# Kernel tuning notes

Hardware: AMD Instinct MI355X
Metric: run time of the kernel (lower is better)

The kernel has to match this reference:

```python
import jax, jax.numpy as jnp
import numpy as np

ALPHA = 0.5  # leakage
T, B, I, H = 512, 64, 128, 1024
SCALE = 0.9  # input_scaling
RHO = 0.99   # target spectral radius (approximated by 1/sqrt(H) normal scaling)


def setup_inputs() -> dict:
    key = jax.random.key(0)
    k1, k2, k3, k4, k5 = jax.random.split(key, 5)
    x = jax.random.normal(k1, (T, B, I), dtype=jnp.float32)
    # uniform(-scale, scale) kernel init
    W_in0 = jax.random.uniform(k2, (H, I), jnp.float32, -SCALE, SCALE)
    # normal recurrent init scaled so spectral radius ~= rho (circular law: radius ~ sigma*sqrt(H))
    W_hat0 = jax.random.normal(k3, (H, H), jnp.float32) * (RHO / np.sqrt(H))
    W_in1 = jax.random.uniform(k4, (H, H), jnp.float32, -SCALE, SCALE)
    W_hat1 = jax.random.normal(k5, (H, H), jnp.float32) * (RHO / np.sqrt(H))
    return {"x": x, "W_in0": W_in0, "W_hat0": W_hat0, "W_in1": W_in1, "W_hat1": W_hat1}


def _run_layer(inp, W_in, W_hat):
    # inp: [T, B, F_in]; returns full state trajectory [T, B, H]
    def step(h, x_t):
        pre = x_t @ W_in.T + h @ W_hat.T          # [B, H]
        h_new = (1.0 - ALPHA) * h + ALPHA * jnp.tanh(pre)
        return h_new, h_new

    h0 = jnp.zeros((inp.shape[1], W_hat.shape[0]), dtype=inp.dtype)
    _, ys = jax.lax.scan(step, h0, inp)
    return ys


def reference(x, W_in0, W_hat0, W_in1, W_hat1):
    e0 = _run_layer(x, W_in0, W_hat0)   # layer 0 states [T, B, H]
    e1 = _run_layer(e0, W_in1, W_hat1)  # layer 1 states [T, B, H]
    return jnp.stack([e0, e1], axis=-2)  # [T, B, num_layers, H]
```

## Files before the change

### kernel.cpp

```cpp
#include <hip/hip_runtime.h>
#include <math.h>

#define TSTEPS 512
#define BATCH  64
#define HDIM   1024
#define IDIM   128
#define NBLOCKS 256
#define NTHR   512

typedef __attribute__((ext_vector_type(8))) short bf16x8;
typedef __attribute__((ext_vector_type(4))) float f32x4;
typedef __attribute__((ext_vector_type(4))) unsigned u32x4;

#define WI0HI 0
#define WI0LO (WI0HI + 1024*128)
#define WH0HI (WI0LO + 1024*128)
#define WH0LO (WH0HI + 1024*1024)
#define WI1HI (WH0LO + 1024*1024)
#define WI1LO (WI1HI + 1024*1024)
#define WH1HI (WI1LO + 1024*1024)
#define WH1LO (WH1HI + 1024*1024)
#define WS_USHORTS (WH1LO + 1024*1024)
#define CNT_OFF_BYTES ((size_t)WS_USHORTS * 2)
#define FLG_DW (256 * 16)
#define BAR_BYTES (2 * 256 * 64)

__device__ __forceinline__ unsigned short bf_hi(float f) {
    unsigned u = __builtin_bit_cast(unsigned, f);
    unsigned r = u + 0x7fffu + ((u >> 16) & 1u);
    return (unsigned short)(r >> 16);
}
__device__ __forceinline__ float bf_tof(unsigned short h) {
    unsigned u = ((unsigned)h) << 16;
    return __builtin_bit_cast(float, u);
}

__device__ __forceinline__ void split8v(f32x4 a, f32x4 b,
                                        bf16x8& ah, bf16x8& al) {
    float fv[8] = {a[0], a[1], a[2], a[3], b[0], b[1], b[2], b[3]};
    u32x4 H, L;
    #pragma unroll
    for (int q = 0; q < 4; ++q) {
        const float f0 = fv[2 * q], f1 = fv[2 * q + 1];
        unsigned h;
        asm("v_cvt_pk_bf16_f32 %0, %1, %2" : "=v"(h) : "v"(f0), "v"(f1));
        const float h0 = __builtin_bit_cast(float, h << 16);
        const float h1 = __builtin_bit_cast(float, h & 0xffff0000u);
        unsigned lo;
        asm("v_cvt_pk_bf16_f32 %0, %1, %2" : "=v"(lo) : "v"(f0 - h0), "v"(f1 - h1));
        H[q] = h; L[q] = lo;
    }
    ah = __builtin_bit_cast(bf16x8, H);
    al = __builtin_bit_cast(bf16x8, L);
}

__device__ __forceinline__ void ks_r2(f32x4 a, f32x4 b,
                                      bf16x8 bh, bf16x8 bl, f32x4& acc) {
    bf16x8 ah, al;
    split8v(a, b, ah, al);
    acc = __builtin_amdgcn_mfma_f32_16x16x32_bf16(ah, bh, acc, 0, 0, 0);
    acc = __builtin_amdgcn_mfma_f32_16x16x32_bf16(al, bh, acc, 0, 0, 0);
    acc = __builtin_amdgcn_mfma_f32_16x16x32_bf16(ah, bl, acc, 0, 0, 0);
}

#define LDG4(B, base, g) _Pragma("unroll") for (int c = 0; c < 4; ++c) { \
    (B)[2*c]   = *(const f32x4*)((base) + ((g)*4 + c) * 32); \
    (B)[2*c+1] = *(const f32x4*)((base) + ((g)*4 + c) * 32 + 4); }
#define PROC4(B, wOff, g) _Pragma("unroll") for (int c = 0; c < 4; ++c) { \
    ks_r2((B)[2*c], (B)[2*c+1], wfh[(wOff)+(g)*4+c], wfl[(wOff)+(g)*4+c], \
          ((((g)*4+c) & 1) ? accA : accB)); }

__global__ void prep_kernel(const float* __restrict__ Wi0, const float* __restrict__ Wh0,
                            const float* __restrict__ Wi1, const float* __restrict__ Wh1,
                            unsigned short* __restrict__ wsU)
{
    const int n = 1024*128 + 3*1024*1024;
    for (int e = blockIdx.x * blockDim.x + threadIdx.x; e < n;
         e += gridDim.x * blockDim.x) {
        const float* src; int idx, hiOff, loOff;
        if (e < 1024*128)            { src = Wi0; idx = e;              hiOff = WI0HI; loOff = WI0LO; }
        else if (e < 1024*128 + 1024*1024)   { src = Wh0; idx = e - 1024*128;   hiOff = WH0HI; loOff = WH0LO; }
        else if (e < 1024*128 + 2*1024*1024) { src = Wi1; idx = e - 1024*128 - 1024*1024; hiOff = WI1HI; loOff = WI1LO; }
        else                         { src = Wh1; idx = e - 1024*128 - 2*1024*1024; hiOff = WH1HI; loOff = WH1LO; }
        float f = src[idx];
        unsigned short h = bf_hi(f);
        wsU[hiOff + idx] = h;
        wsU[loOff + idx] = bf_hi(f - bf_tof(h));
    }
}

__device__ __forceinline__ void barrier_arrive(unsigned* cnt, unsigned epoch) {
    __syncthreads();
    if (threadIdx.x == 0)
        __hip_atomic_store(cnt + (unsigned)blockIdx.x * 16, epoch,
                           __ATOMIC_RELAXED, __HIP_MEMORY_SCOPE_AGENT);
}
__device__ __forceinline__ void barrier_wait(unsigned* cnt, unsigned epoch) {
    const int tid = (int)threadIdx.x;
    if (blockIdx.x == 0) {
        if (tid < 64) {
            unsigned* flg = cnt + FLG_DW;
            for (;;) {
                unsigned v0 = __hip_atomic_load(cnt + (tid      ) * 16, __ATOMIC_RELAXED, __HIP_MEMORY_SCOPE_AGENT);
                unsigned v1 = __hip_atomic_load(cnt + (tid +  64) * 16, __ATOMIC_RELAXED, __HIP_MEMORY_SCOPE_AGENT);
                unsigned v2 = __hip_atomic_load(cnt + (tid + 128) * 16, __ATOMIC_RELAXED, __HIP_MEMORY_SCOPE_AGENT);
                unsigned v3 = __hip_atomic_load(cnt + (tid + 192) * 16, __ATOMIC_RELAXED, __HIP_MEMORY_SCOPE_AGENT);
                bool ok = (v0 >= epoch) & (v1 >= epoch) & (v2 >= epoch) & (v3 >= epoch);
                if (__ballot(ok) == ~0ull) break;
                __builtin_amdgcn_s_sleep(1);
            }
            #pragma unroll
            for (int q = 0; q < 4; ++q)
                __hip_atomic_store(flg + (q * 64 + tid) * 16, epoch,
                                   __ATOMIC_RELAXED, __HIP_MEMORY_SCOPE_AGENT);
        }
    } else if (tid == 0) {
        unsigned* myflag = cnt + FLG_DW + (unsigned)blockIdx.x * 16;
        while (__hip_atomic_load(myflag, __ATOMIC_RELAXED,
                                 __HIP_MEMORY_SCOPE_AGENT) < epoch)
            __builtin_amdgcn_s_sleep(1);
    }
    __syncthreads();
}

__global__ __launch_bounds__(NTHR, 2) void reservoir_kernel(
    const float* __restrict__ x, float* __restrict__ out,
    const unsigned short* __restrict__ wsU, unsigned* __restrict__ cnt)
{
    __shared__ f32x4 red[8 * 64];

    const int bid = blockIdx.x;
    const int layer = bid >> 7;
    const int rr  = bid & 127;
    const int jt  = rr >> 1, mh = rr & 1;
    const int tid = (int)threadIdx.x;
    const int w   = __builtin_amdgcn_readfirstlane(tid >> 6);
    const int m2  = w & 1, kh = w >> 1;
    const int l   = tid & 63, lr = l & 15, tq = l >> 4;
    const int jbase = jt * 16;
    const int arow  = mh * 32 + m2 * 16 + lr;

    bf16x8 wfh[16], wfl[16];
    if (layer == 0) {
        const size_t rx = (size_t)(jbase + lr) * IDIM + kh * 32 + tq * 8;
        wfh[0] = *(const bf16x8*)(wsU + WI0HI + rx);
        wfl[0] = *(const bf16x8*)(wsU + WI0LO + rx);
        const size_t rh = (size_t)(jbase + lr) * HDIM + kh * 256 + tq * 8;
        #pragma unroll
        for (int ks = 0; ks < 8; ++ks) {
            wfh[1 + ks] = *(const bf16x8*)(wsU + WH0HI + rh + ks * 32);
            wfl[1 + ks] = *(const bf16x8*)(wsU + WH0LO + rh + ks * 32);
        }
    } else {
        const int hiOff = (kh < 2) ? WI1HI : WH1HI;
        const int loOff = (kh < 2) ? WI1LO : WH1LO;
        const size_t ro = (size_t)(jbase + lr) * HDIM + (kh & 1) * 512 + tq * 8;
        #pragma unroll
        for (int ks = 0; ks < 16; ++ks) {
            wfh[ks] = *(const bf16x8*)(wsU + hiOff + ro + ks * 32);
            wfl[ks] = *(const bf16x8*)(wsU + loOff + ro + ks * 32);
        }
    }

    float hold[4] = {0.f, 0.f, 0.f, 0.f};
    f32x4 accX = {0.f, 0.f, 0.f, 0.f};

    for (int i = 0; i <= TSTEPS; ++i) {
        const int t = layer ? (i - 1) : i;
        const bool valid = layer ? (t >= 0) : (t < TSTEPS);
        if (valid) {
            f32x4 accA = {0.f, 0.f, 0.f, 0.f};
            f32x4 accB = {0.f, 0.f, 0.f, 0.f};
            if (layer == 0) {
                if (i == 0) {
                    f32x4 xa = *(const f32x4*)(x + (size_t)t * (BATCH * IDIM) + arow * IDIM + kh * 32 + tq * 8);
                    f32x4 xb = *(const f32x4*)(x + (size_t)t * (BATCH * IDIM) + arow * IDIM + kh * 32 + tq * 8 + 4);
                    ks_r2(xa, xb, wfh[0], wfl[0], accA);
                } else {
                    accA = accX;
                }
                if (t >= 1) {
                    const float* h0 = out + (size_t)(t - 1) * 131072 + arow * 2048
                                      + kh * 256 + tq * 8;
                    f32x4 bA[8], bB[8];
                    LDG4(bA, h0, 0);
                    LDG4(bB, h0, 1);
                    PROC4(bA, 1, 0);
                    PROC4(bB, 1, 1);
                }
            } else {
                const bool doit = (kh < 2) || (t >= 1);
                if (doit) {
                    const int ts  = (kh < 2) ? t : (t - 1);
                    const float* src = out + (size_t)ts * 131072 + arow * 2048
                                       + ((kh < 2) ? 0 : 1024) + (kh & 1) * 512 + tq * 8;
                    f32x4 bA[8], bB[8];
                    LDG4(bA, src, 0);
                    LDG4(bB, src, 1);
                    PROC4(bA, 0, 0);
                    LDG4(bA, src, 2);
                    PROC4(bB, 0, 1);
                    LDG4(bB, src, 3);
                    PROC4(bA, 0, 2);
                    PROC4(bB, 0, 3);
                }
            }

            red[w * 64 + l] = accA + accB;
            __syncthreads();
            if (w < 2) {
                f32x4 s  = red[(w + 0) * 64 + l];
                f32x4 s1 = red[(w + 2) * 64 + l];
                f32x4 s2 = red[(w + 4) * 64 + l];
                f32x4 s3 = red[(w + 6) * 64 + l];
                #pragma unroll
                for (int r = 0; r < 4; ++r) {
                    const float pre = ((s[r] + s1[r]) + (s2[r] + s3[r]));
                    const float hnew = 0.5f * hold[r] + 0.5f * tanhf(pre);
                    hold[r] = hnew;
                    const int row = mh * 32 + w * 16 + tq * 4 + r;
                    const int col = jbase + lr;
                    float* dst = out + (size_t)t * 131072 + row * 2048 + layer * 1024 + col;
                    __hip_atomic_store(dst, hnew, __ATOMIC_RELAXED, __HIP_MEMORY_SCOPE_AGENT);
                }
            }
            __syncthreads();
        }
        if (i < TSTEPS) {
            barrier_arrive(cnt, (unsigned)(i + 1));
            if (layer == 0 && (i + 1) < TSTEPS) {
                const float* xs = x + (size_t)(i + 1) * (BATCH * IDIM) + arow * IDIM + kh * 32 + tq * 8;
                f32x4 xa = *(const f32x4*)(xs);
                f32x4 xb = *(const f32x4*)(xs + 4);
                f32x4 z = {0.f, 0.f, 0.f, 0.f};
                ks_r2(xa, xb, wfh[0], wfl[0], z);
                accX = z;
            }
            barrier_wait(cnt, (unsigned)(i + 1));
        }
    }
}

extern "C" void kernel_launch(void* const* d_in, const int* in_sizes, int n_in,
                              void* d_out, int out_size, void* d_ws, size_t ws_size,
                              hipStream_t stream) {
    const float* x   = (const float*)d_in[0];
    const float* Wi0 = (const float*)d_in[1];
    const float* Wh0 = (const float*)d_in[2];
    const float* Wi1 = (const float*)d_in[3];
    const float* Wh1 = (const float*)d_in[4];
    float* out = (float*)d_out;
    unsigned short* wsU = (unsigned short*)d_ws;
    unsigned* cnt = (unsigned*)((char*)d_ws + CNT_OFF_BYTES);

    hipMemsetAsync((char*)d_ws + CNT_OFF_BYTES, 0, BAR_BYTES, stream);
    prep_kernel<<<256, 256, 0, stream>>>(Wi0, Wh0, Wi1, Wh1, wsU);

    void* args[] = {(void*)&x, (void*)&out, (void*)&wsU, (void*)&cnt};
    hipLaunchCooperativeKernel((const void*)reservoir_kernel,
                               dim3(NBLOCKS), dim3(NTHR), args, 0, stream);
}
```

Before: 4.723 ms.

## Split grid barrier per layer and spread epilogue across all threads

Replaces the single global barrier with two per-layer barriers. Block 0 of each layer gathers arrivals only from its own 128 blocks and publishes to a separate flag array. Layer-1 blocks wait on both the layer-0 and layer-1 flags, so layer-0 blocks no longer wait for layer-1 stragglers. The reduction and tanh epilogue now runs on all 512 threads, one output element each, instead of two waves handling four each, which shortens the serial tail of every step. The price is extra flag memory and a more involved dependency protocol between the layers.

```diff
diff --git a/kernel.cpp b/kernel.cpp
--- a/kernel.cpp
+++ b/kernel.cpp
@@ -23,7 +23,7 @@
 #define WS_USHORTS (WH1LO + 1024*1024)
 #define CNT_OFF_BYTES ((size_t)WS_USHORTS * 2)
 #define FLG_DW (256 * 16)
-#define BAR_BYTES (2 * 256 * 64)
+#define BAR_BYTES (3 * 256 * 64)
 
 __device__ __forceinline__ unsigned short bf_hi(float f) {
     unsigned u = __builtin_bit_cast(unsigned, f);
@@ -95,30 +95,46 @@
         __hip_atomic_store(cnt + (unsigned)blockIdx.x * 16, epoch,
                            __ATOMIC_RELAXED, __HIP_MEMORY_SCOPE_AGENT);
 }
-__device__ __forceinline__ void barrier_wait(unsigned* cnt, unsigned epoch) {
+__device__ __forceinline__ void barrier_wait(unsigned* cnt, unsigned epoch, int layer) {
     const int tid = (int)threadIdx.x;
-    if (blockIdx.x == 0) {
+    const int bid = (int)blockIdx.x;
+    if ((bid & 127) == 0) {
         if (tid < 64) {
-            unsigned* flg = cnt + FLG_DW;
+            unsigned* arr = cnt + layer * (128 * 16);
             for (;;) {
-                unsigned v0 = __hip_atomic_load(cnt + (tid      ) * 16, __ATOMIC_RELAXED, __HIP_MEMORY_SCOPE_AGENT);
-                unsigned v1 = __hip_atomic_load(cnt + (tid +  64) * 16, __ATOMIC_RELAXED, __HIP_MEMORY_SCOPE_AGENT);
-                unsigned v2 = __hip_atomic_load(cnt + (tid + 128) * 16, __ATOMIC_RELAXED, __HIP_MEMORY_SCOPE_AGENT);
-                unsigned v3 = __hip_atomic_load(cnt + (tid + 192) * 16, __ATOMIC_RELAXED, __HIP_MEMORY_SCOPE_AGENT);
-                bool ok = (v0 >= epoch) & (v1 >= epoch) & (v2 >= epoch) & (v3 >= epoch);
+                unsigned v0 = __hip_atomic_load(arr + (tid     ) * 16, __ATOMIC_RELAXED, __HIP_MEMORY_SCOPE_AGENT);
+                unsigned v1 = __hip_atomic_load(arr + (tid + 64) * 16, __ATOMIC_RELAXED, __HIP_MEMORY_SCOPE_AGENT);
+                bool ok = (v0 >= epoch) & (v1 >= epoch);
                 if (__ballot(ok) == ~0ull) break;
                 __builtin_amdgcn_s_sleep(1);
             }
+            unsigned* flg = cnt + FLG_DW + layer * 4096;
             #pragma unroll
             for (int q = 0; q < 4; ++q)
                 __hip_atomic_store(flg + (q * 64 + tid) * 16, epoch,
                                    __ATOMIC_RELAXED, __HIP_MEMORY_SCOPE_AGENT);
         }
+        if (layer == 1 && tid == 0) {
+            unsigned* f0 = cnt + FLG_DW + (unsigned)bid * 16;
+            while (__hip_atomic_load(f0, __ATOMIC_RELAXED,
+                                     __HIP_MEMORY_SCOPE_AGENT) < epoch)
+                __builtin_amdgcn_s_sleep(1);
+        }
     } else if (tid == 0) {
-        unsigned* myflag = cnt + FLG_DW + (unsigned)blockIdx.x * 16;
-        while (__hip_atomic_load(myflag, __ATOMIC_RELAXED,
-                                 __HIP_MEMORY_SCOPE_AGENT) < epoch)
-            __builtin_amdgcn_s_sleep(1);
+        unsigned* f0 = cnt + FLG_DW + (unsigned)bid * 16;
+        if (layer == 0) {
+            while (__hip_atomic_load(f0, __ATOMIC_RELAXED,
+                                     __HIP_MEMORY_SCOPE_AGENT) < epoch)
+                __builtin_amdgcn_s_sleep(1);
+        } else {
+            unsigned* f1 = cnt + FLG_DW + 4096 + (unsigned)bid * 16;
+            for (;;) {
+                unsigned a = __hip_atomic_load(f1, __ATOMIC_RELAXED, __HIP_MEMORY_SCOPE_AGENT);
+                unsigned b = __hip_atomic_load(f0, __ATOMIC_RELAXED, __HIP_MEMORY_SCOPE_AGENT);
+                if (a >= epoch && b >= epoch) break;
+                __builtin_amdgcn_s_sleep(1);
+            }
+        }
     }
     __syncthreads();
 }
@@ -162,7 +178,11 @@
         }
     }
 
-    float hold[4] = {0.f, 0.f, 0.f, 0.f};
+    const int rowLocal = tid >> 4;
+    const int colF = tid & 15;
+    const int m2f = rowLocal >> 4, tqf = (rowLocal >> 2) & 3, rf = rowLocal & 3;
+    const int lf  = tqf * 16 + colF;
+    float hold = 0.f;
     f32x4 accX = {0.f, 0.f, 0.f, 0.f};
 
     for (int i = 0; i <= TSTEPS; ++i) {
@@ -208,21 +228,16 @@
 
             red[w * 64 + l] = accA + accB;
             __syncthreads();
-            if (w < 2) {
-                f32x4 s  = red[(w + 0) * 64 + l];
-                f32x4 s1 = red[(w + 2) * 64 + l];
-                f32x4 s2 = red[(w + 4) * 64 + l];
-                f32x4 s3 = red[(w + 6) * 64 + l];
+            {
+                float s = 0.f;
                 #pragma unroll
-                for (int r = 0; r < 4; ++r) {
-                    const float pre = ((s[r] + s1[r]) + (s2[r] + s3[r]));
-                    const float hnew = 0.5f * hold[r] + 0.5f * tanhf(pre);
-                    hold[r] = hnew;
-                    const int row = mh * 32 + w * 16 + tq * 4 + r;
-                    const int col = jbase + lr;
-                    float* dst = out + (size_t)t * 131072 + row * 2048 + layer * 1024 + col;
-                    __hip_atomic_store(dst, hnew, __ATOMIC_RELAXED, __HIP_MEMORY_SCOPE_AGENT);
-                }
+                for (int k4 = 0; k4 < 4; ++k4)
+                    s += red[(k4 * 2 + m2f) * 64 + lf][rf];
+                const float hnew = 0.5f * hold + 0.5f * tanhf(s);
+                hold = hnew;
+                const int row = mh * 32 + rowLocal;
+                float* dst = out + (size_t)t * 131072 + row * 2048 + layer * 1024 + jbase + colF;
+                __hip_atomic_store(dst, hnew, __ATOMIC_RELAXED, __HIP_MEMORY_SCOPE_AGENT);
             }
             __syncthreads();
         }
@@ -236,7 +251,7 @@
                 ks_r2(xa, xb, wfh[0], wfl[0], z);
                 accX = z;
             }
-            barrier_wait(cnt, (unsigned)(i + 1));
+            barrier_wait(cnt, (unsigned)(i + 1), layer);
         }
     }
 }
```

After: 4.620 ms. 1.02x faster.
